# Optimization experiments

Measured on AMD Instinct MI355X. Metric: run time of the kernel, lower is better.

Reference implementation:

```python
import jax, jax.numpy as jnp
import numpy as np

K = 512
D = 64


def setup_inputs() -> dict:
    key = jax.random.key(0)
    k1, k2 = jax.random.split(key)
    z_e_x = jax.random.normal(k1, (32, D, 64, 64), dtype=jnp.float32)  # [B, D, H, W]
    # codebook initialized uniform(-1/K, 1/K) as in the torch module
    emb = jax.random.uniform(k2, (K, D), dtype=jnp.float32, minval=-1.0 / K, maxval=1.0 / K)
    return {"z_e_x": z_e_x, "emb": emb}


def reference(z_e_x, emb):
    B, Dc, H, W = z_e_x.shape
    # [B, D, H, W] -> [B*H*W, D]
    z = jnp.transpose(z_e_x, (0, 2, 3, 1)).reshape(-1, Dc)
    z_norm = jnp.sum(z * z, axis=1, keepdims=True)          # [N, 1]
    e_norm = jnp.sum(emb * emb, axis=1)[None, :]            # [1, K]
    dists = z_norm + e_norm - 2.0 * (z @ emb.T)             # [N, K]
    dists = dists.reshape(B, H, W, -1)
    latents = jnp.argmin(dists, axis=-1)                    # [B, H, W] int
    return latents
```

## Files before the change

kernel.cpp:

```cpp
#include <hip/hip_runtime.h>

#define KCODES 512
#define DDIM   64
#define NROWS  131072

typedef short bf16x8 __attribute__((ext_vector_type(8)));
typedef float f32x4  __attribute__((ext_vector_type(4)));
typedef int   i32x4  __attribute__((ext_vector_type(4)));

union frag_cast { i32x4 i; bf16x8 h; };

__device__ __forceinline__ unsigned f32_to_bf16_rne(float x) {
    unsigned u = __float_as_uint(x);
    return (u + 0x7fffu + ((u >> 16) & 1u)) >> 16;
}

__device__ __forceinline__ void gload16(const void* g, void* l) {
    __builtin_amdgcn_global_load_lds(
        (const __attribute__((address_space(1))) void*)g,
        (__attribute__((address_space(3))) void*)l, 16, 0, 0);
}

__global__ __launch_bounds__(64) void k1_prep(const float* __restrict__ emb,
                                              float* __restrict__ en, float* __restrict__ emaxp,
                                              i32x4* __restrict__ efA, i32x4* __restrict__ efB,
                                              int* __restrict__ cnt) {
    const int kt = blockIdx.x, t = threadIdx.x;
    const int krow = t & 15, gq = t >> 4;
    const int k = kt * 16 + krow;

    float er[16];
    float pz = 0.f;
#pragma unroll
    for (int c = 0; c < 2; ++c)
#pragma unroll
        for (int j = 0; j < 8; ++j) {
            float x = emb[k * DDIM + c * 32 + gq * 8 + j];
            er[c * 8 + j] = x;
            pz = fmaf(x, x, pz);
        }

#pragma unroll
    for (int c = 0; c < 2; ++c) {
        unsigned hh[8], hl[8];
#pragma unroll
        for (int j = 0; j < 8; ++j) {
            float x = er[c * 8 + j];
            unsigned h = f32_to_bf16_rne(x);
            float hf = __uint_as_float(h << 16);
            hh[j] = h;
            hl[j] = f32_to_bf16_rne(x - hf);
        }
        i32x4 wh, wl;
#pragma unroll
        for (int i = 0; i < 4; ++i) {
            wh[i] = (int)(hh[2 * i] | (hh[2 * i + 1] << 16));
            wl[i] = (int)(hl[2 * i] | (hl[2 * i + 1] << 16));
        }
        int idx = (kt * 2 + c) * 64 + krow + 16 * gq;
        efA[idx] = wh;
        efB[idx] = wl;
    }

    pz += __shfl_xor(pz, 16);
    pz += __shfl_xor(pz, 32);
    if (t < 16) en[k] = pz;

    float m = pz;
#pragma unroll
    for (int sh = 1; sh <= 8; sh <<= 1) m = fmaxf(m, __shfl_xor(m, sh));
    if (t == 0) {
        emaxp[kt] = m;
        if (kt == 0) cnt[0] = 0;
    }
}

__global__ __launch_bounds__(256, 4) void k3_fused(
    const float* __restrict__ z,
    const i32x4* __restrict__ efA_, const i32x4* __restrict__ efB_,
    const float* __restrict__ en_g, float* __restrict__ zn_g,
    const float* __restrict__ emaxp, int* __restrict__ out,
    int* __restrict__ list, int* __restrict__ cnt) {

    __shared__ i32x4 sfrag[4][2][4][64];
    __shared__ float en_l[KCODES];
    __shared__ float zn_l[128];

    const int t = threadIdx.x, blk = blockIdx.x;
    const int n0 = blk * 128;
    const int b = n0 >> 12, hw0 = n0 & 4095;
    const int w = t >> 6, lane = t & 63;
    const int klane = lane & 15, g = lane >> 4;

    en_l[t] = en_g[t];
    en_l[t + 256] = en_g[t + 256];

    float em2 = 0.f;
#pragma unroll
    for (int i = 0; i < 32; ++i) em2 = fmaxf(em2, emaxp[i]);
    const float emax = sqrtf(em2) * 1.0001f;

    const float* zbase = z + (size_t)b * (DDIM * 4096) + hw0;
    bf16x8 zh[2][2], zl[2][2];
#pragma unroll
    for (int tl = 0; tl < 2; ++tl) {
        const int row = w * 32 + tl * 16 + klane;
        float zv[16];
#pragma unroll
        for (int c = 0; c < 2; ++c)
#pragma unroll
            for (int j = 0; j < 8; ++j)
                zv[c * 8 + j] = zbase[(size_t)(c * 32 + g * 8 + j) * 4096 + row];
        float pz = 0.f;
#pragma unroll
        for (int c = 0; c < 2; ++c) {
            unsigned hh[8], hl[8];
#pragma unroll
            for (int j = 0; j < 8; ++j) {
                float x = zv[c * 8 + j];
                pz = fmaf(x, x, pz);
                unsigned h = f32_to_bf16_rne(x);
                float hf = __uint_as_float(h << 16);
                hh[j] = h;
                hl[j] = f32_to_bf16_rne(x - hf);
            }
            frag_cast uh, ul;
#pragma unroll
            for (int i = 0; i < 4; ++i) {
                uh.i[i] = (int)(hh[2 * i] | (hh[2 * i + 1] << 16));
                ul.i[i] = (int)(hl[2 * i] | (hl[2 * i + 1] << 16));
            }
            zh[tl][c] = uh.h;
            zl[tl][c] = ul.h;
        }
        pz += __shfl_xor(pz, 16);
        pz += __shfl_xor(pz, 32);
        if (g == 0) {
            zn_l[w * 32 + tl * 16 + klane] = pz;
            zn_g[n0 + w * 32 + tl * 16 + klane] = pz;
        }
    }
    __syncthreads();

    f32x4 zn4[2];
    zn4[0] = *(const f32x4*)&zn_l[w * 32 + g * 4];
    zn4[1] = *(const f32x4*)&zn_l[w * 32 + 16 + g * 4];

    float m1[2][4], m2[2][4];
    int i1[2][4];
#pragma unroll
    for (int tl = 0; tl < 2; ++tl)
#pragma unroll
        for (int r = 0; r < 4; ++r) { m1[tl][r] = 3.4e38f; m2[tl][r] = 3.4e38f; i1[tl][r] = 0; }

    f32x4 zero = {0.f, 0.f, 0.f, 0.f};

    auto issue = [&](int kt, int buf) {
        const i32x4* gA = efA_ + kt * 128 + lane;
        const i32x4* gB = efB_ + kt * 128 + lane;
        gload16(gA,      &sfrag[w][buf][0][0]);
        gload16(gA + 64, &sfrag[w][buf][1][0]);
        gload16(gB,      &sfrag[w][buf][2][0]);
        gload16(gB + 64, &sfrag[w][buf][3][0]);
    };

    issue(0, 0);
    issue(1, 1);

#pragma unroll 1
    for (int kt = 0; kt < 32; ++kt) {
        const int buf = kt & 1;
        if (kt < 31) { asm volatile("s_waitcnt vmcnt(4)" ::: "memory"); }
        else         { asm volatile("s_waitcnt vmcnt(0)" ::: "memory"); }

        frag_cast e0h, e1h, e0l, e1l;
        e0h.i = sfrag[w][buf][0][lane];
        e1h.i = sfrag[w][buf][1][lane];
        e0l.i = sfrag[w][buf][2][lane];
        e1l.i = sfrag[w][buf][3][lane];
        asm volatile("s_waitcnt lgkmcnt(0)" ::: "memory");
        __builtin_amdgcn_sched_barrier(0);
        if (kt < 30) issue(kt + 2, buf);

        const int k = kt * 16 + klane;
        const float enk = en_l[k];
#pragma unroll
        for (int tl = 0; tl < 2; ++tl) {
            f32x4 acc = __builtin_amdgcn_mfma_f32_16x16x32_bf16(zh[tl][0], e0h.h, zero, 0, 0, 0);
            acc = __builtin_amdgcn_mfma_f32_16x16x32_bf16(zh[tl][1], e1h.h, acc, 0, 0, 0);
            acc = __builtin_amdgcn_mfma_f32_16x16x32_bf16(zh[tl][0], e0l.h, acc, 0, 0, 0);
            acc = __builtin_amdgcn_mfma_f32_16x16x32_bf16(zh[tl][1], e1l.h, acc, 0, 0, 0);
            acc = __builtin_amdgcn_mfma_f32_16x16x32_bf16(zl[tl][0], e0h.h, acc, 0, 0, 0);
            acc = __builtin_amdgcn_mfma_f32_16x16x32_bf16(zl[tl][1], e1h.h, acc, 0, 0, 0);
#pragma unroll
            for (int r = 0; r < 4; ++r) {
                float d = fmaf(-2.f, acc[r], zn4[tl][r] + enk);
                float o1 = m1[tl][r];
                i1[tl][r] = (d < o1) ? k : i1[tl][r];
                m2[tl][r] = fminf(m2[tl][r], fmaxf(o1, d));
                m1[tl][r] = fminf(o1, d);
            }
        }
    }

#pragma unroll
    for (int sh = 1; sh <= 8; sh <<= 1) {
#pragma unroll
        for (int tl = 0; tl < 2; ++tl)
#pragma unroll
            for (int r = 0; r < 4; ++r) {
                float om1 = __shfl_xor(m1[tl][r], sh);
                int oi1 = __shfl_xor(i1[tl][r], sh);
                float om2 = __shfl_xor(m2[tl][r], sh);
                float hi = fmaxf(m1[tl][r], om1);
                m2[tl][r] = fminf(fminf(m2[tl][r], om2), hi);
                i1[tl][r] = (om1 < m1[tl][r]) ? oi1 : i1[tl][r];
                m1[tl][r] = fminf(m1[tl][r], om1);
            }
    }

    if (klane == 0) {
#pragma unroll
        for (int tl = 0; tl < 2; ++tl) {
            int rowbase = n0 + w * 32 + tl * 16 + g * 4;
            i32x4 idx4;
#pragma unroll
            for (int r = 0; r < 4; ++r) idx4[r] = i1[tl][r];
            *(i32x4*)(out + rowbase) = idx4;
#pragma unroll
            for (int r = 0; r < 4; ++r) {
                float zz = zn4[tl][r];
                float W = fmaf(sqrtf(zz) * emax, 1.0e-4f, zz * 1.0e-6f);
                if (m2[tl][r] - m1[tl][r] <= W) {
                    int pos = atomicAdd(cnt, 1);
                    list[pos] = rowbase + r;
                }
            }
        }
    }
}

__global__ __launch_bounds__(256) void k4_refine(
    const float* __restrict__ z, const float* __restrict__ emb,
    const float* __restrict__ en, const float* __restrict__ zn_g,
    const int* __restrict__ list, const int* __restrict__ cnt,
    int* __restrict__ out) {
    __shared__ float zrow[4][64];
    int t = threadIdx.x;
    int w = t >> 6, lane = t & 63;
    int nlist = cnt[0];
    for (int li = blockIdx.x * 4 + w; li < nlist; li += gridDim.x * 4) {
        int row = list[li];
        int b = row >> 12, hw = row & 4095;
        const float* zp = z + (size_t)b * (DDIM * 4096) + hw;
        zrow[w][lane] = zp[(size_t)lane * 4096];
        float zn = zn_g[row];
        float best = 3.4e38f;
        int bi = 0;
#pragma unroll 1
        for (int kk = 0; kk < 8; ++kk) {
            int k = lane * 8 + kk;
            const float* e0 = emb + k * DDIM;
            float acc = 0.f;
#pragma unroll
            for (int d = 0; d < DDIM; ++d) acc = fmaf(e0[d], zrow[w][d], acc);
            float dist = fmaf(-2.f, acc, zn + en[k]);
            if (dist < best) { best = dist; bi = k; }
        }
        unsigned long long key =
            ((unsigned long long)__float_as_uint(best) << 32) | (unsigned)bi;
#pragma unroll
        for (int sh = 32; sh; sh >>= 1) {
            unsigned long long o = __shfl_xor(key, sh);
            key = (o < key) ? o : key;
        }
        if (lane == 0) out[row] = (int)(key & 0xFFFFFFFFull);
    }
}

__global__ void fb_enorm(const float* __restrict__ emb, float* __restrict__ en) {
    int k = blockIdx.x * blockDim.x + threadIdx.x;
    if (k < KCODES) {
        float s = 0.f;
#pragma unroll
        for (int d = 0; d < DDIM; ++d) { float e = emb[k * DDIM + d]; s = fmaf(e, e, s); }
        en[k] = s;
    }
}
__global__ __launch_bounds__(256) void fb_argmin(const float* __restrict__ z,
                                                 const float* __restrict__ emb,
                                                 const float* __restrict__ en,
                                                 int* __restrict__ out, int nrows) {
    int n = blockIdx.x * blockDim.x + threadIdx.x;
    if (n >= nrows) return;
    int b = n >> 12, hw = n & 4095;
    const float* zp = z + (size_t)b * (DDIM * 4096) + hw;
    float zr[DDIM];
#pragma unroll
    for (int d = 0; d < DDIM; ++d) zr[d] = zp[(size_t)d * 4096];
    float zn = 0.f;
#pragma unroll
    for (int d = 0; d < DDIM; ++d) zn = fmaf(zr[d], zr[d], zn);
    float best = 3.4e38f; int bi = 0;
    for (int k0 = 0; k0 < KCODES; k0 += 8) {
        float acc[8];
#pragma unroll
        for (int kk = 0; kk < 8; ++kk) acc[kk] = 0.f;
        const float* e0 = emb + k0 * DDIM;
#pragma unroll
        for (int d = 0; d < DDIM; ++d) {
            float zd = zr[d];
#pragma unroll
            for (int kk = 0; kk < 8; ++kk) acc[kk] = fmaf(e0[kk * DDIM + d], zd, acc[kk]);
        }
#pragma unroll
        for (int kk = 0; kk < 8; ++kk) {
            float dist = fmaf(-2.f, acc[kk], zn + en[k0 + kk]);
            if (dist < best) { best = dist; bi = k0 + kk; }
        }
    }
    out[n] = bi;
}

extern "C" void kernel_launch(void* const* d_in, const int* in_sizes, int n_in,
                              void* d_out, int out_size, void* d_ws, size_t ws_size,
                              hipStream_t stream) {
    const float* z   = (const float*)d_in[0];
    const float* emb = (const float*)d_in[1];
    int* out = (int*)d_out;

    const size_t SZ_EF   = 32 * 2 * 64 * 16;
    const size_t SZ_EN   = KCODES * 4;
    const size_t SZ_ZN   = (size_t)NROWS * 4;
    const size_t SZ_EMAX = 128;
    const size_t SZ_LIST = (size_t)NROWS * 4;
    const size_t SZ_CNT  = 64;
    const size_t NEED = 2 * SZ_EF + SZ_EN + SZ_ZN + SZ_EMAX + SZ_LIST + SZ_CNT;

    if (ws_size < NEED) {
        float* en = (float*)d_ws;
        fb_enorm<<<2, 256, 0, stream>>>(emb, en);
        fb_argmin<<<NROWS / 256, 256, 0, stream>>>(z, emb, en, out, NROWS);
        return;
    }

    char* p = (char*)d_ws;
    i32x4* efA = (i32x4*)p;   p += SZ_EF;
    i32x4* efB = (i32x4*)p;   p += SZ_EF;
    float* en  = (float*)p;   p += SZ_EN;
    float* zn  = (float*)p;   p += SZ_ZN;
    float* emaxp = (float*)p; p += SZ_EMAX;
    int* list = (int*)p;      p += SZ_LIST;
    int* cnt  = (int*)p;

    k1_prep<<<32, 64, 0, stream>>>(emb, en, emaxp, efA, efB, cnt);
    k3_fused<<<NROWS / 128, 256, 0, stream>>>(z, efA, efB, en, zn, emaxp, out, list, cnt);
    k4_refine<<<512, 256, 0, stream>>>(z, emb, en, zn, list, cnt, out);
}
```

Measured before the change: 87.30 us.

## Fuse refinement into main kernel and share codebook tiles across 8 waves

```diff
diff --git a/kernel.cpp b/kernel.cpp
--- a/kernel.cpp
+++ b/kernel.cpp
@@ -23,8 +23,7 @@
 
 __global__ __launch_bounds__(64) void k1_prep(const float* __restrict__ emb,
                                               float* __restrict__ en, float* __restrict__ emaxp,
-                                              i32x4* __restrict__ efA, i32x4* __restrict__ efB,
-                                              int* __restrict__ cnt) {
+                                              i32x4* __restrict__ efP) {
     const int kt = blockIdx.x, t = threadIdx.x;
     const int krow = t & 15, gq = t >> 4;
     const int k = kt * 16 + krow;
@@ -57,9 +56,8 @@
             wh[i] = (int)(hh[2 * i] | (hh[2 * i + 1] << 16));
             wl[i] = (int)(hl[2 * i] | (hl[2 * i + 1] << 16));
         }
-        int idx = (kt * 2 + c) * 64 + krow + 16 * gq;
-        efA[idx] = wh;
-        efB[idx] = wl;
+        efP[kt * 256 + c * 64 + krow + 16 * gq]       = wh;
+        efP[kt * 256 + (2 + c) * 64 + krow + 16 * gq] = wl;
     }
 
     pz += __shfl_xor(pz, 16);
@@ -69,22 +67,21 @@
     float m = pz;
 #pragma unroll
     for (int sh = 1; sh <= 8; sh <<= 1) m = fmaxf(m, __shfl_xor(m, sh));
-    if (t == 0) {
-        emaxp[kt] = m;
-        if (kt == 0) cnt[0] = 0;
-    }
-}
-
-__global__ __launch_bounds__(256, 4) void k3_fused(
-    const float* __restrict__ z,
-    const i32x4* __restrict__ efA_, const i32x4* __restrict__ efB_,
-    const float* __restrict__ en_g, float* __restrict__ zn_g,
-    const float* __restrict__ emaxp, int* __restrict__ out,
-    int* __restrict__ list, int* __restrict__ cnt) {
-
-    __shared__ i32x4 sfrag[4][2][4][64];
+    if (t == 0) emaxp[kt] = m;
+}
+
+__global__ __launch_bounds__(512, 8) void k3_fused(
+    const float* __restrict__ z, const float* __restrict__ emb,
+    const i32x4* __restrict__ efP,
+    const float* __restrict__ en_g, const float* __restrict__ emaxp,
+    int* __restrict__ out) {
+
+    __shared__ i32x4 sfrag[3][4][64];
     __shared__ float en_l[KCODES];
     __shared__ float zn_l[128];
+    __shared__ float zrow_s[8][64];
+    __shared__ int   flag_rows[128];
+    __shared__ int   nflag;
 
     const int t = threadIdx.x, blk = blockIdx.x;
     const int n0 = blk * 128;
@@ -92,8 +89,15 @@
     const int w = t >> 6, lane = t & 63;
     const int klane = lane & 15, g = lane >> 4;
 
-    en_l[t] = en_g[t];
-    en_l[t + 256] = en_g[t + 256];
+    if (t == 0) nflag = 0;
+
+    if (w < 4) {
+        gload16(efP + 0 * 256 + w * 64 + lane, &sfrag[0][w][0]);
+        gload16(efP + 1 * 256 + w * 64 + lane, &sfrag[1][w][0]);
+    }
+
+    en_l[t] = (t < KCODES) ? en_g[t] : 0.f;
+    if (t < KCODES - 512 + 512) {}
 
     float em2 = 0.f;
 #pragma unroll
@@ -101,10 +105,9 @@
     const float emax = sqrtf(em2) * 1.0001f;
 
     const float* zbase = z + (size_t)b * (DDIM * 4096) + hw0;
-    bf16x8 zh[2][2], zl[2][2];
-#pragma unroll
-    for (int tl = 0; tl < 2; ++tl) {
-        const int row = w * 32 + tl * 16 + klane;
+    const int row = w * 16 + klane;
+    bf16x8 zh[2], zl[2];
+    {
         float zv[16];
 #pragma unroll
         for (int c = 0; c < 2; ++c)
@@ -130,131 +133,99 @@
                 uh.i[i] = (int)(hh[2 * i] | (hh[2 * i + 1] << 16));
                 ul.i[i] = (int)(hl[2 * i] | (hl[2 * i + 1] << 16));
             }
-            zh[tl][c] = uh.h;
-            zl[tl][c] = ul.h;
+            zh[c] = uh.h;
+            zl[c] = ul.h;
         }
         pz += __shfl_xor(pz, 16);
         pz += __shfl_xor(pz, 32);
-        if (g == 0) {
-            zn_l[w * 32 + tl * 16 + klane] = pz;
-            zn_g[n0 + w * 32 + tl * 16 + klane] = pz;
-        }
+        if (g == 0) zn_l[w * 16 + klane] = pz;
     }
     __syncthreads();
 
-    f32x4 zn4[2];
-    zn4[0] = *(const f32x4*)&zn_l[w * 32 + g * 4];
-    zn4[1] = *(const f32x4*)&zn_l[w * 32 + 16 + g * 4];
-
-    float m1[2][4], m2[2][4];
-    int i1[2][4];
-#pragma unroll
-    for (int tl = 0; tl < 2; ++tl)
-#pragma unroll
-        for (int r = 0; r < 4; ++r) { m1[tl][r] = 3.4e38f; m2[tl][r] = 3.4e38f; i1[tl][r] = 0; }
+    f32x4 zn4 = *(const f32x4*)&zn_l[w * 16 + g * 4];
+
+    float m1[4], m2[4];
+    int i1[4];
+#pragma unroll
+    for (int r = 0; r < 4; ++r) { m1[r] = 3.4e38f; m2[r] = 3.4e38f; i1[r] = 0; }
 
     f32x4 zero = {0.f, 0.f, 0.f, 0.f};
 
-    auto issue = [&](int kt, int buf) {
-        const i32x4* gA = efA_ + kt * 128 + lane;
-        const i32x4* gB = efB_ + kt * 128 + lane;
-        gload16(gA,      &sfrag[w][buf][0][0]);
-        gload16(gA + 64, &sfrag[w][buf][1][0]);
-        gload16(gB,      &sfrag[w][buf][2][0]);
-        gload16(gB + 64, &sfrag[w][buf][3][0]);
-    };
-
-    issue(0, 0);
-    issue(1, 1);
-
+    int buf = 0;
 #pragma unroll 1
     for (int kt = 0; kt < 32; ++kt) {
-        const int buf = kt & 1;
-        if (kt < 31) { asm volatile("s_waitcnt vmcnt(4)" ::: "memory"); }
+        if (kt < 31) { asm volatile("s_waitcnt vmcnt(1)" ::: "memory"); }
         else         { asm volatile("s_waitcnt vmcnt(0)" ::: "memory"); }
+        __builtin_amdgcn_s_barrier();
+        if (w < 4 && kt + 2 < 32) {
+            int ibuf = buf + 2; if (ibuf >= 3) ibuf -= 3;
+            gload16(efP + (size_t)(kt + 2) * 256 + w * 64 + lane, &sfrag[ibuf][w][0]);
+        }
 
         frag_cast e0h, e1h, e0l, e1l;
-        e0h.i = sfrag[w][buf][0][lane];
-        e1h.i = sfrag[w][buf][1][lane];
-        e0l.i = sfrag[w][buf][2][lane];
-        e1l.i = sfrag[w][buf][3][lane];
+        e0h.i = sfrag[buf][0][lane];
+        e1h.i = sfrag[buf][1][lane];
+        e0l.i = sfrag[buf][2][lane];
+        e1l.i = sfrag[buf][3][lane];
         asm volatile("s_waitcnt lgkmcnt(0)" ::: "memory");
         __builtin_amdgcn_sched_barrier(0);
-        if (kt < 30) issue(kt + 2, buf);
 
         const int k = kt * 16 + klane;
         const float enk = en_l[k];
-#pragma unroll
-        for (int tl = 0; tl < 2; ++tl) {
-            f32x4 acc = __builtin_amdgcn_mfma_f32_16x16x32_bf16(zh[tl][0], e0h.h, zero, 0, 0, 0);
-            acc = __builtin_amdgcn_mfma_f32_16x16x32_bf16(zh[tl][1], e1h.h, acc, 0, 0, 0);
-            acc = __builtin_amdgcn_mfma_f32_16x16x32_bf16(zh[tl][0], e0l.h, acc, 0, 0, 0);
-            acc = __builtin_amdgcn_mfma_f32_16x16x32_bf16(zh[tl][1], e1l.h, acc, 0, 0, 0);
-            acc = __builtin_amdgcn_mfma_f32_16x16x32_bf16(zl[tl][0], e0h.h, acc, 0, 0, 0);
-            acc = __builtin_amdgcn_mfma_f32_16x16x32_bf16(zl[tl][1], e1h.h, acc, 0, 0, 0);
-#pragma unroll
-            for (int r = 0; r < 4; ++r) {
-                float d = fmaf(-2.f, acc[r], zn4[tl][r] + enk);
-                float o1 = m1[tl][r];
-                i1[tl][r] = (d < o1) ? k : i1[tl][r];
-                m2[tl][r] = fminf(m2[tl][r], fmaxf(o1, d));
-                m1[tl][r] = fminf(o1, d);
+        f32x4 acc = __builtin_amdgcn_mfma_f32_16x16x32_bf16(zh[0], e0h.h, zero, 0, 0, 0);
+        acc = __builtin_amdgcn_mfma_f32_16x16x32_bf16(zh[1], e1h.h, acc, 0, 0, 0);
+        acc = __builtin_amdgcn_mfma_f32_16x16x32_bf16(zh[0], e0l.h, acc, 0, 0, 0);
+        acc = __builtin_amdgcn_mfma_f32_16x16x32_bf16(zh[1], e1l.h, acc, 0, 0, 0);
+        acc = __builtin_amdgcn_mfma_f32_16x16x32_bf16(zl[0], e0h.h, acc, 0, 0, 0);
+        acc = __builtin_amdgcn_mfma_f32_16x16x32_bf16(zl[1], e1h.h, acc, 0, 0, 0);
+#pragma unroll
+        for (int r = 0; r < 4; ++r) {
+            float d = fmaf(-2.f, acc[r], zn4[r] + enk);
+            float o1 = m1[r];
+            i1[r] = (d < o1) ? k : i1[r];
+            m2[r] = fminf(m2[r], fmaxf(o1, d));
+            m1[r] = fminf(o1, d);
+        }
+        buf = (buf + 1 == 3) ? 0 : buf + 1;
+    }
+
+#pragma unroll
+    for (int sh = 1; sh <= 8; sh <<= 1) {
+#pragma unroll
+        for (int r = 0; r < 4; ++r) {
+            float om1 = __shfl_xor(m1[r], sh);
+            int oi1 = __shfl_xor(i1[r], sh);
+            float om2 = __shfl_xor(m2[r], sh);
+            float hi = fmaxf(m1[r], om1);
+            m2[r] = fminf(fminf(m2[r], om2), hi);
+            i1[r] = (om1 < m1[r]) ? oi1 : i1[r];
+            m1[r] = fminf(m1[r], om1);
+        }
+    }
+
+    if (klane == 0) {
+        int rowbase = n0 + w * 16 + g * 4;
+        i32x4 idx4;
+#pragma unroll
+        for (int r = 0; r < 4; ++r) idx4[r] = i1[r];
+        *(i32x4*)(out + rowbase) = idx4;
+#pragma unroll
+        for (int r = 0; r < 4; ++r) {
+            float zz = zn4[r];
+            float W = fmaf(sqrtf(zz) * emax, 1.0e-4f, zz * 1.0e-6f);
+            if (m2[r] - m1[r] <= W) {
+                int p = atomicAdd(&nflag, 1);
+                flag_rows[p] = w * 16 + g * 4 + r;
             }
         }
     }
-
-#pragma unroll
-    for (int sh = 1; sh <= 8; sh <<= 1) {
-#pragma unroll
-        for (int tl = 0; tl < 2; ++tl)
-#pragma unroll
-            for (int r = 0; r < 4; ++r) {
-                float om1 = __shfl_xor(m1[tl][r], sh);
-                int oi1 = __shfl_xor(i1[tl][r], sh);
-                float om2 = __shfl_xor(m2[tl][r], sh);
-                float hi = fmaxf(m1[tl][r], om1);
-                m2[tl][r] = fminf(fminf(m2[tl][r], om2), hi);
-                i1[tl][r] = (om1 < m1[tl][r]) ? oi1 : i1[tl][r];
-                m1[tl][r] = fminf(m1[tl][r], om1);
-            }
-    }
-
-    if (klane == 0) {
-#pragma unroll
-        for (int tl = 0; tl < 2; ++tl) {
-            int rowbase = n0 + w * 32 + tl * 16 + g * 4;
-            i32x4 idx4;
-#pragma unroll
-            for (int r = 0; r < 4; ++r) idx4[r] = i1[tl][r];
-            *(i32x4*)(out + rowbase) = idx4;
-#pragma unroll
-            for (int r = 0; r < 4; ++r) {
-                float zz = zn4[tl][r];
-                float W = fmaf(sqrtf(zz) * emax, 1.0e-4f, zz * 1.0e-6f);
-                if (m2[tl][r] - m1[tl][r] <= W) {
-                    int pos = atomicAdd(cnt, 1);
-                    list[pos] = rowbase + r;
-                }
-            }
-        }
-    }
-}
-
-__global__ __launch_bounds__(256) void k4_refine(
-    const float* __restrict__ z, const float* __restrict__ emb,
-    const float* __restrict__ en, const float* __restrict__ zn_g,
-    const int* __restrict__ list, const int* __restrict__ cnt,
-    int* __restrict__ out) {
-    __shared__ float zrow[4][64];
-    int t = threadIdx.x;
-    int w = t >> 6, lane = t & 63;
-    int nlist = cnt[0];
-    for (int li = blockIdx.x * 4 + w; li < nlist; li += gridDim.x * 4) {
-        int row = list[li];
-        int b = row >> 12, hw = row & 4095;
-        const float* zp = z + (size_t)b * (DDIM * 4096) + hw;
-        zrow[w][lane] = zp[(size_t)lane * 4096];
-        float zn = zn_g[row];
+    __syncthreads();
+
+    const int nf = nflag;
+    for (int i = w; i < nf; i += 8) {
+        const int lrow = flag_rows[i];
+        zrow_s[w][lane] = zbase[(size_t)lane * 4096 + lrow];
+        const float znr = zn_l[lrow];
         float best = 3.4e38f;
         int bi = 0;
 #pragma unroll 1
@@ -263,8 +234,8 @@
             const float* e0 = emb + k * DDIM;
             float acc = 0.f;
 #pragma unroll
-            for (int d = 0; d < DDIM; ++d) acc = fmaf(e0[d], zrow[w][d], acc);
-            float dist = fmaf(-2.f, acc, zn + en[k]);
+            for (int d = 0; d < DDIM; ++d) acc = fmaf(e0[d], zrow_s[w][d], acc);
+            float dist = fmaf(-2.f, acc, znr + en_l[k]);
             if (dist < best) { best = dist; bi = k; }
         }
         unsigned long long key =
@@ -274,7 +245,7 @@
             unsigned long long o = __shfl_xor(key, sh);
             key = (o < key) ? o : key;
         }
-        if (lane == 0) out[row] = (int)(key & 0xFFFFFFFFull);
+        if (lane == 0) out[n0 + lrow] = (int)(key & 0xFFFFFFFFull);
     }
 }
 
@@ -329,13 +300,10 @@
     const float* emb = (const float*)d_in[1];
     int* out = (int*)d_out;
 
-    const size_t SZ_EF   = 32 * 2 * 64 * 16;
+    const size_t SZ_EF   = 32 * 4 * 64 * 16;
     const size_t SZ_EN   = KCODES * 4;
-    const size_t SZ_ZN   = (size_t)NROWS * 4;
     const size_t SZ_EMAX = 128;
-    const size_t SZ_LIST = (size_t)NROWS * 4;
-    const size_t SZ_CNT  = 64;
-    const size_t NEED = 2 * SZ_EF + SZ_EN + SZ_ZN + SZ_EMAX + SZ_LIST + SZ_CNT;
+    const size_t NEED = SZ_EF + SZ_EN + SZ_EMAX;
 
     if (ws_size < NEED) {
         float* en = (float*)d_ws;
@@ -345,15 +313,10 @@
     }
 
     char* p = (char*)d_ws;
-    i32x4* efA = (i32x4*)p;   p += SZ_EF;
-    i32x4* efB = (i32x4*)p;   p += SZ_EF;
+    i32x4* efP = (i32x4*)p;   p += SZ_EF;
     float* en  = (float*)p;   p += SZ_EN;
-    float* zn  = (float*)p;   p += SZ_ZN;
-    float* emaxp = (float*)p; p += SZ_EMAX;
-    int* list = (int*)p;      p += SZ_LIST;
-    int* cnt  = (int*)p;
-
-    k1_prep<<<32, 64, 0, stream>>>(emb, en, emaxp, efA, efB, cnt);
-    k3_fused<<<NROWS / 128, 256, 0, stream>>>(z, efA, efB, en, zn, emaxp, out, list, cnt);
-    k4_refine<<<512, 256, 0, stream>>>(z, emb, en, zn, list, cnt, out);
-}
+    float* emaxp = (float*)p;
+
+    k1_prep<<<32, 64, 0, stream>>>(emb, en, emaxp, efP);
+    k3_fused<<<NROWS / 128, 512, 0, stream>>>(z, emb, efP, en, emaxp, out);
+}
```

Measured after the change: 96.30 us. 1.1x slower.

## Fuse exact refine pass into main argmin kernel using per-block shared flag list

Applied to the files above, without the earlier changes.

```diff
diff --git a/kernel.cpp b/kernel.cpp
--- a/kernel.cpp
+++ b/kernel.cpp
@@ -23,8 +23,7 @@
 
 __global__ __launch_bounds__(64) void k1_prep(const float* __restrict__ emb,
                                               float* __restrict__ en, float* __restrict__ emaxp,
-                                              i32x4* __restrict__ efA, i32x4* __restrict__ efB,
-                                              int* __restrict__ cnt) {
+                                              i32x4* __restrict__ efA, i32x4* __restrict__ efB) {
     const int kt = blockIdx.x, t = threadIdx.x;
     const int krow = t & 15, gq = t >> 4;
     const int k = kt * 16 + krow;
@@ -69,28 +68,28 @@
     float m = pz;
 #pragma unroll
     for (int sh = 1; sh <= 8; sh <<= 1) m = fmaxf(m, __shfl_xor(m, sh));
-    if (t == 0) {
-        emaxp[kt] = m;
-        if (kt == 0) cnt[0] = 0;
-    }
+    if (t == 0) emaxp[kt] = m;
 }
 
 __global__ __launch_bounds__(256, 4) void k3_fused(
-    const float* __restrict__ z,
+    const float* __restrict__ z, const float* __restrict__ emb,
     const i32x4* __restrict__ efA_, const i32x4* __restrict__ efB_,
-    const float* __restrict__ en_g, float* __restrict__ zn_g,
-    const float* __restrict__ emaxp, int* __restrict__ out,
-    int* __restrict__ list, int* __restrict__ cnt) {
+    const float* __restrict__ en_g, const float* __restrict__ emaxp,
+    int* __restrict__ out) {
 
     __shared__ i32x4 sfrag[4][2][4][64];
     __shared__ float en_l[KCODES];
     __shared__ float zn_l[128];
+    __shared__ int   flag_rows[128];
+    __shared__ int   nflag;
 
     const int t = threadIdx.x, blk = blockIdx.x;
     const int n0 = blk * 128;
     const int b = n0 >> 12, hw0 = n0 & 4095;
     const int w = t >> 6, lane = t & 63;
     const int klane = lane & 15, g = lane >> 4;
+
+    if (t == 0) nflag = 0;
 
     en_l[t] = en_g[t];
     en_l[t + 256] = en_g[t + 256];
@@ -135,16 +134,9 @@
         }
         pz += __shfl_xor(pz, 16);
         pz += __shfl_xor(pz, 32);
-        if (g == 0) {
-            zn_l[w * 32 + tl * 16 + klane] = pz;
-            zn_g[n0 + w * 32 + tl * 16 + klane] = pz;
-        }
+        if (g == 0) zn_l[w * 32 + tl * 16 + klane] = pz;
     }
     __syncthreads();
-
-    f32x4 zn4[2];
-    zn4[0] = *(const f32x4*)&zn_l[w * 32 + g * 4];
-    zn4[1] = *(const f32x4*)&zn_l[w * 32 + 16 + g * 4];
 
     float m1[2][4], m2[2][4];
     int i1[2][4];
@@ -194,7 +186,7 @@
             acc = __builtin_amdgcn_mfma_f32_16x16x32_bf16(zl[tl][1], e1h.h, acc, 0, 0, 0);
 #pragma unroll
             for (int r = 0; r < 4; ++r) {
-                float d = fmaf(-2.f, acc[r], zn4[tl][r] + enk);
+                float d = fmaf(-2.f, acc[r], enk);
                 float o1 = m1[tl][r];
                 i1[tl][r] = (d < o1) ? k : i1[tl][r];
                 m2[tl][r] = fminf(m2[tl][r], fmaxf(o1, d));
@@ -229,32 +221,23 @@
             *(i32x4*)(out + rowbase) = idx4;
 #pragma unroll
             for (int r = 0; r < 4; ++r) {
-                float zz = zn4[tl][r];
+                float zz = zn_l[w * 32 + tl * 16 + g * 4 + r];
                 float W = fmaf(sqrtf(zz) * emax, 1.0e-4f, zz * 1.0e-6f);
                 if (m2[tl][r] - m1[tl][r] <= W) {
-                    int pos = atomicAdd(cnt, 1);
-                    list[pos] = rowbase + r;
+                    int p = atomicAdd(&nflag, 1);
+                    flag_rows[p] = w * 32 + tl * 16 + g * 4 + r;
                 }
             }
         }
     }
-}
-
-__global__ __launch_bounds__(256) void k4_refine(
-    const float* __restrict__ z, const float* __restrict__ emb,
-    const float* __restrict__ en, const float* __restrict__ zn_g,
-    const int* __restrict__ list, const int* __restrict__ cnt,
-    int* __restrict__ out) {
-    __shared__ float zrow[4][64];
-    int t = threadIdx.x;
-    int w = t >> 6, lane = t & 63;
-    int nlist = cnt[0];
-    for (int li = blockIdx.x * 4 + w; li < nlist; li += gridDim.x * 4) {
-        int row = list[li];
-        int b = row >> 12, hw = row & 4095;
-        const float* zp = z + (size_t)b * (DDIM * 4096) + hw;
-        zrow[w][lane] = zp[(size_t)lane * 4096];
-        float zn = zn_g[row];
+    __syncthreads();
+
+    float (*zrow_s)[64] = (float(*)[64])&sfrag[0][0][0][0];
+    const int nf = nflag;
+    for (int i = w; i < nf; i += 4) {
+        const int lrow = flag_rows[i];
+        zrow_s[w][lane] = zbase[(size_t)lane * 4096 + lrow];
+        const float znr = zn_l[lrow];
         float best = 3.4e38f;
         int bi = 0;
 #pragma unroll 1
@@ -263,8 +246,8 @@
             const float* e0 = emb + k * DDIM;
             float acc = 0.f;
 #pragma unroll
-            for (int d = 0; d < DDIM; ++d) acc = fmaf(e0[d], zrow[w][d], acc);
-            float dist = fmaf(-2.f, acc, zn + en[k]);
+            for (int d = 0; d < DDIM; ++d) acc = fmaf(e0[d], zrow_s[w][d], acc);
+            float dist = fmaf(-2.f, acc, znr + en_l[k]);
             if (dist < best) { best = dist; bi = k; }
         }
         unsigned long long key =
@@ -274,7 +257,7 @@
             unsigned long long o = __shfl_xor(key, sh);
             key = (o < key) ? o : key;
         }
-        if (lane == 0) out[row] = (int)(key & 0xFFFFFFFFull);
+        if (lane == 0) out[n0 + lrow] = (int)(key & 0xFFFFFFFFull);
     }
 }
 
@@ -331,11 +314,8 @@
 
     const size_t SZ_EF   = 32 * 2 * 64 * 16;
     const size_t SZ_EN   = KCODES * 4;
-    const size_t SZ_ZN   = (size_t)NROWS * 4;
     const size_t SZ_EMAX = 128;
-    const size_t SZ_LIST = (size_t)NROWS * 4;
-    const size_t SZ_CNT  = 64;
-    const size_t NEED = 2 * SZ_EF + SZ_EN + SZ_ZN + SZ_EMAX + SZ_LIST + SZ_CNT;
+    const size_t NEED = 2 * SZ_EF + SZ_EN + SZ_EMAX;
 
     if (ws_size < NEED) {
         float* en = (float*)d_ws;
@@ -348,12 +328,8 @@
     i32x4* efA = (i32x4*)p;   p += SZ_EF;
     i32x4* efB = (i32x4*)p;   p += SZ_EF;
     float* en  = (float*)p;   p += SZ_EN;
-    float* zn  = (float*)p;   p += SZ_ZN;
-    float* emaxp = (float*)p; p += SZ_EMAX;
-    int* list = (int*)p;      p += SZ_LIST;
-    int* cnt  = (int*)p;
-
-    k1_prep<<<32, 64, 0, stream>>>(emb, en, emaxp, efA, efB, cnt);
-    k3_fused<<<NROWS / 128, 256, 0, stream>>>(z, efA, efB, en, zn, emaxp, out, list, cnt);
-    k4_refine<<<512, 256, 0, stream>>>(z, emb, en, zn, list, cnt, out);
-}
+    float* emaxp = (float*)p;
+
+    k1_prep<<<32, 64, 0, stream>>>(emb, en, emaxp, efA, efB);
+    k3_fused<<<NROWS / 128, 256, 0, stream>>>(z, emb, efA, efB, en, emaxp, out);
+}
```

Result: faster. 78.54 us (-10.0%).
